# Optimization experiments

Measured on AMD Instinct MI355X. Metric: run time of the kernel, lower is better.

Reference implementation:

```python
import jax, jax.numpy as jnp
import numpy as np

N = 20000      # nodes
E = 320000     # edges (avg degree 16)
IN = 128
HID = 64
CLS = 32
H0, H1, H2 = 4, 4, 6
SLOPE = 0.2


def _lin(key, fan_in, fan_out):
    kw, kb = jax.random.split(key)
    s = 1.0 / np.sqrt(fan_in)
    W = jax.random.uniform(kw, (fan_in, fan_out), minval=-s, maxval=s, dtype=jnp.float32)
    b = jax.random.uniform(kb, (fan_out,), minval=-s, maxval=s, dtype=jnp.float32)
    return W, b


def setup_inputs() -> dict:
    key = jax.random.key(0)
    ks = jax.random.split(key, 16)
    x = jax.random.normal(ks[0], (N, IN), dtype=jnp.float32)
    src = jax.random.randint(ks[1], (E,), 0, N)
    dst = jax.random.randint(ks[2], (E,), 0, N)
    W0s, b0s = _lin(ks[3], IN, H0 * HID)
    W0d, b0d = _lin(ks[4], IN, H0 * HID)
    a0 = jax.random.normal(ks[5], (H0, HID), dtype=jnp.float32) * 0.05
    d1 = H0 * HID  # 256, flattened hidden width
    W1s, b1s = _lin(ks[6], d1, H1 * HID)
    W1d, b1d = _lin(ks[7], d1, H1 * HID)
    a1 = jax.random.normal(ks[8], (H1, HID), dtype=jnp.float32) * 0.05
    W2s, b2s = _lin(ks[9], d1, H2 * CLS)
    W2d, b2d = _lin(ks[10], d1, H2 * CLS)
    a2 = jax.random.normal(ks[11], (H2, CLS), dtype=jnp.float32) * 0.05
    Wr2, br2 = _lin(ks[12], d1, H2 * CLS)  # residual projection (256 != 192)
    return dict(x=x, src=src, dst=dst,
                W0s=W0s, b0s=b0s, W0d=W0d, b0d=b0d, a0=a0,
                W1s=W1s, b1s=b1s, W1d=W1d, b1d=b1d, a1=a1,
                W2s=W2s, b2s=b2s, W2d=W2d, b2d=b2d, a2=a2,
                Wr2=Wr2, br2=br2)


def _gatv2_layer(x, src, dst, Ws, bs, Wd, bd, attn, heads, dim, res, act):
    n = x.shape[0]
    feat_src = (x @ Ws + bs).reshape(n, heads, dim)
    feat_dst = (x @ Wd + bd).reshape(n, heads, dim)
    # GATv2 edge scores: a^T LeakyReLU(W_l h_u + W_r h_v)
    e = jax.nn.leaky_relu(feat_src[src] + feat_dst[dst], SLOPE)  # [E,H,D]
    logits = jnp.einsum('ehd,hd->eh', e, attn)                    # [E,H]
    # numerically-stable edge softmax over incoming edges per destination
    m = jax.ops.segment_max(logits, dst, num_segments=n)
    m = jnp.where(jnp.isfinite(m), m, 0.0)
    ex = jnp.exp(logits - m[dst])
    denom = jax.ops.segment_sum(ex, dst, num_segments=n)
    alpha = ex / denom[dst]                                        # [E,H]
    out = jax.ops.segment_sum(feat_src[src] * alpha[:, :, None], dst, num_segments=n)
    if res == 'id':
        out = out + x.reshape(n, heads, dim)
    elif res is not None:
        Wr, br = res
        out = out + (x @ Wr + br).reshape(n, heads, dim)
    if act:
        out = jax.nn.elu(out)
    return out  # [n, heads, dim]


def reference(x, src, dst,
              W0s, b0s, W0d, b0d, a0,
              W1s, b1s, W1d, b1d, a1,
              W2s, b2s, W2d, b2d, a2,
              Wr2, br2):
    h = _gatv2_layer(x, src, dst, W0s, b0s, W0d, b0d, a0, H0, HID, None, True)
    h = h.reshape(N, H0 * HID)
    h = _gatv2_layer(h, src, dst, W1s, b1s, W1d, b1d, a1, H1, HID, 'id', True)
    h = h.reshape(N, H1 * HID)
    out = _gatv2_layer(h, src, dst, W2s, b2s, W2d, b2d, a2, H2, CLS, (Wr2, br2), False)
    return out.mean(axis=1)  # [N, num_classes]
```

## Files before the change

### kernel.cpp

```cpp
#include <hip/hip_runtime.h>
#include <hip/hip_bf16.h>
#include <float.h>
#include <math.h>

#define NN 20000
#define EE 320000
#define IN_DIM 128
#define SLOPE_ 0.2f
#define DEG_CAP 64

typedef __attribute__((ext_vector_type(4))) float f32x4;
typedef _Float16 f16;
typedef __attribute__((ext_vector_type(2))) _Float16 f16x2;
typedef __attribute__((ext_vector_type(4))) _Float16 f16x4;
typedef __attribute__((ext_vector_type(8))) _Float16 f16x8;
typedef unsigned short ushort;

__device__ inline void prep_elem(const float* __restrict__ Wa, const float* __restrict__ ba, int na,
                                 const float* __restrict__ Wb, const float* __restrict__ bb, int nb,
                                 const float* __restrict__ Wc, const float* __restrict__ bc, int nc,
                                 int K, f16* __restrict__ Wt, float* __restrict__ bias_cat, int idx) {
    int n = idx / K;
    int k = idx - n * K;
    const float* W; const float* b; int nl; int ncols;
    if (n < na) { W = Wa; b = ba; nl = n; ncols = na; }
    else if (n < na + nb) { W = Wb; b = bb; nl = n - na; ncols = nb; }
    else { W = Wc; b = bc; nl = n - na - nb; ncols = nc; }
    Wt[(size_t)n * K + k] = (f16)W[(size_t)k * ncols + nl];
    if (k == 0) bias_cat[n] = b[nl];
}

#define SEG0 (512 * 128)
#define SEG1 (512 * 256)
#define SEG2 (576 * 256)
#define SEG3 (NN * IN_DIM / 4)
#define SEG4 (EE)
__global__ void prep_all(const float* __restrict__ W0s, const float* __restrict__ b0s,
                         const float* __restrict__ W0d, const float* __restrict__ b0d,
                         const float* __restrict__ W1s, const float* __restrict__ b1s,
                         const float* __restrict__ W1d, const float* __restrict__ b1d,
                         const float* __restrict__ W2s, const float* __restrict__ b2s,
                         const float* __restrict__ W2d, const float* __restrict__ b2d,
                         const float* __restrict__ Wr2, const float* __restrict__ br2,
                         const float* __restrict__ x,
                         const int* __restrict__ src, const int* __restrict__ dst,
                         f16* __restrict__ Wt0, float* __restrict__ bias0,
                         f16* __restrict__ Wt1, float* __restrict__ bias1,
                         f16* __restrict__ Wt2, float* __restrict__ bias2,
                         f16* __restrict__ A, unsigned int* __restrict__ deg,
                         int* __restrict__ csr_src) {
    int idx = blockIdx.x * 256 + threadIdx.x;
    if (idx < SEG0) {
        prep_elem(W0s, b0s, 256, W0d, b0d, 256, nullptr, nullptr, 0, 128, Wt0, bias0, idx);
    } else if ((idx -= SEG0) < SEG1) {
        prep_elem(W1s, b1s, 256, W1d, b1d, 256, nullptr, nullptr, 0, 256, Wt1, bias1, idx);
    } else if ((idx -= SEG1) < SEG2) {
        prep_elem(W2s, b2s, 192, W2d, b2d, 192, Wr2, br2, 192, 256, Wt2, bias2, idx);
    } else if ((idx -= SEG2) < SEG3) {
        float4 v = ((const float4*)x)[idx];
        f16x4 o = {(f16)v.x, (f16)v.y, (f16)v.z, (f16)v.w};
        ((f16x4*)A)[idx] = o;
    } else if ((idx -= SEG3) < SEG4) {
        int d = dst[idx];
        unsigned int pos = atomicAdd(&deg[d], 1u);
        csr_src[(unsigned)d * DEG_CAP + pos] = src[idx];
    }
}

__global__ __launch_bounds__(256) void gemm_mfma_f16(
        const f16* __restrict__ A, const f16* __restrict__ Wt,
        const float* __restrict__ bias,
        f16* __restrict__ F0, f16* __restrict__ F1, float* __restrict__ F2,
        int b1, int b2, int M, int K, int S, int gx, int gy) {
    __shared__ f16 Bs[64 * 256];
    __shared__ f16 Cs[4][32 * 66];

    const int bid = blockIdx.x;
    const int p = bid & 7;
    const int q = bid >> 3;
    const int bn_i = q % gx;
    const int bm_i = (q / gx) * 8 + p;
    if (bm_i >= gy) return;
    const int bm = bm_i * 256;
    const int bn = bn_i * 64;

    const int tid = threadIdx.x;
    const int wave = tid >> 6;
    const int lane = tid & 63;
    const int m16 = lane & 15;
    const int quad = lane >> 4;

    {
        const int n = tid >> 2;
        const int q0 = tid & 3;
        for (int j = 0; j * 32 < K; ++j) {
            int k0 = j * 32 + q0 * 8;
            f16x8 v = *(const f16x8*)(Wt + (size_t)(bn + n) * K + k0);
            int chunk = (j * 4 + (n >> 4)) * 64 + q0 * 16 + (n & 15);
            *(f16x8*)&Bs[chunk * 8] = v;
        }
    }
    __syncthreads();

    const int rb0 = bm + wave * 64;
    f32x4 acc[2][2][4];
    #pragma unroll
    for (int mi = 0; mi < 2; ++mi)
        #pragma unroll
        for (int mt = 0; mt < 2; ++mt)
            #pragma unroll
            for (int nt = 0; nt < 4; ++nt) acc[mi][mt][nt] = (f32x4){0.f, 0.f, 0.f, 0.f};

    int ar[2][2];
    #pragma unroll
    for (int mi = 0; mi < 2; ++mi)
        #pragma unroll
        for (int mt = 0; mt < 2; ++mt) {
            int row = rb0 + mi * 32 + mt * 16 + m16;
            ar[mi][mt] = row < M ? row : M - 1;
        }

    #pragma unroll 2
    for (int k0 = 0; k0 < K; k0 += 32) {
        f16x8 bs[4];
        #pragma unroll
        for (int nt = 0; nt < 4; ++nt)
            bs[nt] = *(const f16x8*)&Bs[(((k0 >> 5) * 4 + nt) * 64 + lane) * 8];
        #pragma unroll
        for (int mi = 0; mi < 2; ++mi) {
            f16x8 ah[2];
            #pragma unroll
            for (int mt = 0; mt < 2; ++mt)
                ah[mt] = *(const f16x8*)(A + (size_t)ar[mi][mt] * K + k0 + quad * 8);
            #pragma unroll
            for (int nt = 0; nt < 4; ++nt)
                #pragma unroll
                for (int mt = 0; mt < 2; ++mt)
                    acc[mi][mt][nt] = __builtin_amdgcn_mfma_f32_16x16x32_f16(ah[mt], bs[nt], acc[mi][mt][nt], 0, 0, 0);
        }
    }

    #pragma unroll
    for (int mi = 0; mi < 2; ++mi) {
        const int rbase = rb0 + mi * 32;
        if (bn < b2) {
            f16* __restrict__ Fb;
            int cs, cb;
            if (bn >= b1) { Fb = F1; cb = bn - b1; cs = b2 - b1; }
            else          { Fb = F0; cb = bn;      cs = b1; }
            f16* cw = &Cs[wave][0];
            #pragma unroll
            for (int nt = 0; nt < 4; ++nt) {
                float bv = bias[bn + nt * 16 + m16];
                #pragma unroll
                for (int mt = 0; mt < 2; ++mt)
                    #pragma unroll
                    for (int r = 0; r < 4; ++r) {
                        int row = mt * 16 + quad * 4 + r;
                        cw[row * 66 + nt * 16 + m16] = (f16)(acc[mi][mt][nt][r] + bv);
                    }
            }
            int lrow = lane >> 1;
            int lcol = (lane & 1) * 32;
            int grow = rbase + lrow;
            if (grow < M) {
                #pragma unroll
                for (int j = 0; j < 4; ++j) {
                    f16x8 v = *(f16x8*)&cw[lrow * 66 + lcol + j * 8];
                    *(f16x8*)&Fb[(size_t)grow * cs + cb + lcol + j * 8] = v;
                }
            }
        } else {
            int cs = S - b2;
            #pragma unroll
            for (int nt = 0; nt < 4; ++nt) {
                int col = bn - b2 + nt * 16 + m16;
                float bv = bias[bn + nt * 16 + m16];
                #pragma unroll
                for (int mt = 0; mt < 2; ++mt)
                    #pragma unroll
                    for (int r = 0; r < 4; ++r) {
                        int row = rbase + mt * 16 + quad * 4 + r;
                        if (row < M) F2[(size_t)row * cs + col] = acc[mi][mt][nt][r] + bv;
                    }
            }
        }
    }
}

#define AGG_STEP4(U0)                                                         \
    _Pragma("unroll")                                                         \
    for (int uu = 0; uu < 4; ++uu) {                                          \
        const int u = (U0) + uu;                                              \
        const f16x8 cur = buf[u];                                             \
        buf[u] = *(const f16x8*)&fsb[(unsigned)cidx[u] * HD + off];           \
        cidx[u] = csr_src[min(jj0 + b + 16 + u, last)];                       \
        float p = 0.f;                                                        \
        _Pragma("unroll")                                                     \
        for (int i = 0; i < 4; ++i) {                                         \
            f16x2 cp = (f16x2){cur[2 * i], cur[2 * i + 1]};                   \
            f16x2 xp = cp + fdp[i];                                           \
            unsigned xu = __builtin_bit_cast(unsigned, xp) & 0x7FFF7FFFu;     \
            f16x2 xa = __builtin_bit_cast(f16x2, xu);                         \
            p = __builtin_amdgcn_fdot2(xp, a6p[i], p, false);                 \
            p = __builtin_amdgcn_fdot2(xa, a4p[i], p, false);                 \
        }                                                                     \
        _Pragma("unroll")                                                     \
        for (int o = 1; o < GSZ; o <<= 1) p += __shfl_xor(p, o, 64);          \
        float w = (b + u < deg) ? __expf(p) : 0.f;                            \
        lh += w;                                                              \
        _Pragma("unroll")                                                     \
        for (int d = 0; d < 8; ++d) acc[d] += w * (float)cur[d];              \
    }

template <int HD, int D, bool HAS_RES, bool DO_ELU, int OUT_MODE>
__global__ __launch_bounds__(256) void gat_node_aggregate(
        const f16* __restrict__ fsb, const f16* __restrict__ fdb,
        const float* __restrict__ attn,
        const unsigned int* __restrict__ degv,
        const int* __restrict__ csr_src,
        const float* __restrict__ resid, int RS,
        float* __restrict__ outF, f16* __restrict__ outA) {
    constexpr int LANES = HD / 8;
    constexpr int GSZ = D / 8;
    __shared__ float red[(OUT_MODE == 2) ? 8 : 1][(OUT_MODE == 2) ? HD : 1];

    const int wave = threadIdx.x >> 6;
    const int lane = threadIdx.x & 63;
    const int half = lane >> 5;
    const int ln = lane & 31;
    const int t = blockIdx.x * 8 + wave * 2 + half;
    const bool active = (ln < LANES);
    const unsigned off = active ? 8u * ln : 0u;

    f16x2 fdp[4], a6p[4], a4p[4];
    if (active) {
        f16x8 dv = *(const f16x8*)&fdb[(unsigned)t * HD + off];
        float4 aA = *(const float4*)&attn[off];
        float4 aB = *(const float4*)&attn[off + 4];
        float av[8] = {aA.x, aA.y, aA.z, aA.w, aB.x, aB.y, aB.z, aB.w};
        #pragma unroll
        for (int i = 0; i < 4; ++i) {
            fdp[i] = (f16x2){dv[2 * i], dv[2 * i + 1]};
            a6p[i] = (f16x2){(f16)(0.6f * av[2 * i]), (f16)(0.6f * av[2 * i + 1])};
            a4p[i] = (f16x2){(f16)(0.4f * av[2 * i]), (f16)(0.4f * av[2 * i + 1])};
        }
    } else {
        #pragma unroll
        for (int i = 0; i < 4; ++i) {
            fdp[i] = (f16x2){0, 0};
            a6p[i] = (f16x2){0, 0};
            a4p[i] = (f16x2){0, 0};
        }
    }

    const int jj0 = t * DEG_CAP;
    const int deg = (int)degv[t];
    const int last = jj0 + deg - 1;
    const int degO = __shfl_xor(deg, 32, 64);
    const int mdeg = max(deg, degO);

    float acc[8];
    #pragma unroll
    for (int d = 0; d < 8; ++d) acc[d] = 0.f;
    float lh = 0.f;

    f16x8 buf[8];
    int cidx[8];
    #pragma unroll
    for (int u = 0; u < 8; ++u) {
        int e0 = max(min(jj0 + u, last), 0);
        buf[u] = *(const f16x8*)&fsb[(unsigned)csr_src[e0] * HD + off];
        cidx[u] = csr_src[max(min(jj0 + 8 + u, last), 0)];
    }

    for (int b = 0; b < mdeg; b += 8) {
        AGG_STEP4(0)
        if (b + 4 < mdeg) {
            AGG_STEP4(4)
        }
    }

    float inv = (lh > 0.f) ? 1.f / lh : 0.f;
    float vout[8];
    #pragma unroll
    for (int d = 0; d < 8; ++d) vout[d] = acc[d] * inv;
    if (HAS_RES && active) {
        float4 rA = *(const float4*)&resid[(unsigned)t * RS + off];
        float4 rB = *(const float4*)&resid[(unsigned)t * RS + off + 4];
        vout[0] += rA.x; vout[1] += rA.y; vout[2] += rA.z; vout[3] += rA.w;
        vout[4] += rB.x; vout[5] += rB.y; vout[6] += rB.z; vout[7] += rB.w;
    }
    if (DO_ELU) {
        #pragma unroll
        for (int d = 0; d < 8; ++d) vout[d] = vout[d] > 0.f ? vout[d] : expm1f(vout[d]);
    }

    if (OUT_MODE == 2) {
        const int nib = wave * 2 + half;
        if (active) {
            *(float4*)&red[nib][off] = make_float4(vout[0], vout[1], vout[2], vout[3]);
            *(float4*)&red[nib][off + 4] = make_float4(vout[4], vout[5], vout[6], vout[7]);
        }
        __syncthreads();
        int node = threadIdx.x >> 5;
        int col = threadIdx.x & 31;
        float ssum = 0.f;
        #pragma unroll
        for (int h = 0; h < 6; ++h) ssum += red[node][h * 32 + col];
        outF[(unsigned)(blockIdx.x * 8 + node) * 32 + col] = ssum * (1.f / 6.f);
    } else if (active) {
        f16x8 av;
        #pragma unroll
        for (int d = 0; d < 8; ++d) av[d] = (f16)vout[d];
        *(f16x8*)&outA[(unsigned)t * HD + off] = av;
        if (OUT_MODE == 0) {
            *(float4*)&outF[(unsigned)t * HD + off] = make_float4(vout[0], vout[1], vout[2], vout[3]);
            *(float4*)&outF[(unsigned)t * HD + off + 4] = make_float4(vout[4], vout[5], vout[6], vout[7]);
        }
    }
}

extern "C" void kernel_launch(void* const* d_in, const int* in_sizes, int n_in,
                              void* d_out, int out_size, void* d_ws, size_t ws_size,
                              hipStream_t stream) {
    const float* x   = (const float*)d_in[0];
    const int*   src = (const int*)d_in[1];
    const int*   dst = (const int*)d_in[2];
    const float* W0s = (const float*)d_in[3];
    const float* b0s = (const float*)d_in[4];
    const float* W0d = (const float*)d_in[5];
    const float* b0d = (const float*)d_in[6];
    const float* a0  = (const float*)d_in[7];
    const float* W1s = (const float*)d_in[8];
    const float* b1s = (const float*)d_in[9];
    const float* W1d = (const float*)d_in[10];
    const float* b1d = (const float*)d_in[11];
    const float* a1  = (const float*)d_in[12];
    const float* W2s = (const float*)d_in[13];
    const float* b2s = (const float*)d_in[14];
    const float* W2d = (const float*)d_in[15];
    const float* b2d = (const float*)d_in[16];
    const float* a2  = (const float*)d_in[17];
    const float* Wr2 = (const float*)d_in[18];
    const float* br2 = (const float*)d_in[19];

    f16* FsH = (f16*)d_ws;
    f16* FdH = FsH + (size_t)NN * 256;
    f16* A   = FdH + (size_t)NN * 256;
    float* O0 = (float*)(A + (size_t)NN * 256);
    f16* Wt0 = (f16*)(O0 + (size_t)NN * 256);
    f16* Wt1 = Wt0 + 512 * 128;
    f16* Wt2 = Wt1 + 512 * 256;
    float* bias0 = (float*)(Wt2 + 576 * 256);
    float* bias1 = bias0 + 512;
    float* bias2 = bias1 + 512;
    unsigned int* deg = (unsigned int*)(bias2 + 576);
    int* csr_src      = (int*)(deg + NN);

    hipMemsetAsync(deg, 0, (size_t)NN * 4 + (size_t)NN * DEG_CAP * 4, stream);

    {
        int total = SEG0 + SEG1 + SEG2 + SEG3 + SEG4;
        prep_all<<<(total + 255) / 256, 256, 0, stream>>>(
            W0s, b0s, W0d, b0d, W1s, b1s, W1d, b1d, W2s, b2s, W2d, b2d, Wr2, br2, x,
            src, dst, Wt0, bias0, Wt1, bias1, Wt2, bias2, A, deg, csr_src);
    }

    const int gy = (NN + 255) / 256;
    const int gy8 = ((gy + 7) / 8) * 8;
    const int nagg = NN / 8;

    gemm_mfma_f16<<<gy8 * 8, 256, 0, stream>>>(A, Wt0, bias0,
                                               FsH, FdH, nullptr, 256, 512, NN, 128, 512, 8, gy);
    gat_node_aggregate<256, 64, false, true, 0><<<nagg, 256, 0, stream>>>(
        FsH, FdH, a0, deg, csr_src, nullptr, 0, O0, A);

    gemm_mfma_f16<<<gy8 * 8, 256, 0, stream>>>(A, Wt1, bias1,
                                               FsH, FdH, nullptr, 256, 512, NN, 256, 512, 8, gy);
    gat_node_aggregate<256, 64, true, true, 1><<<nagg, 256, 0, stream>>>(
        FsH, FdH, a1, deg, csr_src, O0, 256, nullptr, A);

    gemm_mfma_f16<<<gy8 * 9, 256, 0, stream>>>(A, Wt2, bias2,
                                               FsH, FdH, O0, 192, 384, NN, 256, 576, 9, gy);
    gat_node_aggregate<192, 32, true, false, 2><<<nagg, 256, 0, stream>>>(
        FsH, FdH, a2, deg, csr_src, O0, 192, (float*)d_out, nullptr);
}
```

Measured before the change: 285.3 us.

## Give each aggregation node a full wave, alias GEMM staging LDS, shrink memset

```diff
diff --git a/kernel.cpp b/kernel.cpp
--- a/kernel.cpp
+++ b/kernel.cpp
@@ -6,7 +6,6 @@
 #define NN 20000
 #define EE 320000
 #define IN_DIM 128
-#define SLOPE_ 0.2f
 #define DEG_CAP 64
 
 typedef __attribute__((ext_vector_type(4))) float f32x4;
@@ -14,12 +13,11 @@
 typedef __attribute__((ext_vector_type(2))) _Float16 f16x2;
 typedef __attribute__((ext_vector_type(4))) _Float16 f16x4;
 typedef __attribute__((ext_vector_type(8))) _Float16 f16x8;
-typedef unsigned short ushort;
-
-__device__ inline void prep_elem(const float* __restrict__ Wa, const float* __restrict__ ba, int na,
-                                 const float* __restrict__ Wb, const float* __restrict__ bb, int nb,
-                                 const float* __restrict__ Wc, const float* __restrict__ bc, int nc,
-                                 int K, f16* __restrict__ Wt, float* __restrict__ bias_cat, int idx) {
+
+__device__ __forceinline__ void prep_elem(const float* __restrict__ Wa, const float* __restrict__ ba, int na,
+                                          const float* __restrict__ Wb, const float* __restrict__ bb, int nb,
+                                          const float* __restrict__ Wc, const float* __restrict__ bc, int nc,
+                                          int K, f16* __restrict__ Wt, float* __restrict__ bias_cat, int idx) {
     int n = idx / K;
     int k = idx - n * K;
     const float* W; const float* b; int nl; int ncols;
@@ -63,17 +61,16 @@
     } else if ((idx -= SEG3) < SEG4) {
         int d = dst[idx];
         unsigned int pos = atomicAdd(&deg[d], 1u);
-        csr_src[(unsigned)d * DEG_CAP + pos] = src[idx];
-    }
-}
-
-__global__ __launch_bounds__(256) void gemm_mfma_f16(
+        if (pos < DEG_CAP) csr_src[(unsigned)d * DEG_CAP + pos] = src[idx];
+    }
+}
+
+__global__ __launch_bounds__(256, 4) void gemm_mfma_f16(
         const f16* __restrict__ A, const f16* __restrict__ Wt,
         const float* __restrict__ bias,
         f16* __restrict__ F0, f16* __restrict__ F1, float* __restrict__ F2,
         int b1, int b2, int M, int K, int S, int gx, int gy) {
     __shared__ f16 Bs[64 * 256];
-    __shared__ f16 Cs[4][32 * 66];
 
     const int bid = blockIdx.x;
     const int p = bid & 7;
@@ -140,6 +137,9 @@
         }
     }
 
+    __syncthreads();
+    f16* Cs = Bs;
+
     #pragma unroll
     for (int mi = 0; mi < 2; ++mi) {
         const int rbase = rb0 + mi * 32;
@@ -148,7 +148,7 @@
             int cs, cb;
             if (bn >= b1) { Fb = F1; cb = bn - b1; cs = b2 - b1; }
             else          { Fb = F0; cb = bn;      cs = b1; }
-            f16* cw = &Cs[wave][0];
+            f16* cw = Cs + wave * (32 * 66);
             #pragma unroll
             for (int nt = 0; nt < 4; ++nt) {
                 float bv = bias[bn + nt * 16 + m16];
@@ -192,25 +192,26 @@
     _Pragma("unroll")                                                         \
     for (int uu = 0; uu < 4; ++uu) {                                          \
         const int u = (U0) + uu;                                              \
-        const f16x8 cur = buf[u];                                             \
-        buf[u] = *(const f16x8*)&fsb[(unsigned)cidx[u] * HD + off];           \
-        cidx[u] = csr_src[min(jj0 + b + 16 + u, last)];                       \
-        float p = 0.f;                                                        \
+        const f16x4 cur = buf[u];                                             \
+        unsigned su = (unsigned)cidx[u]; su = su < NN ? su : 0u;              \
+        buf[u] = *(const f16x4*)&fsb[su * (unsigned)HD + off];                \
+        cidx[u] = csr_src[max(min(jj0 + b + 16 + u, last), 0)];               \
+        float pp = 0.f;                                                       \
         _Pragma("unroll")                                                     \
-        for (int i = 0; i < 4; ++i) {                                         \
+        for (int i = 0; i < 2; ++i) {                                         \
             f16x2 cp = (f16x2){cur[2 * i], cur[2 * i + 1]};                   \
             f16x2 xp = cp + fdp[i];                                           \
             unsigned xu = __builtin_bit_cast(unsigned, xp) & 0x7FFF7FFFu;     \
             f16x2 xa = __builtin_bit_cast(f16x2, xu);                         \
-            p = __builtin_amdgcn_fdot2(xp, a6p[i], p, false);                 \
-            p = __builtin_amdgcn_fdot2(xa, a4p[i], p, false);                 \
+            pp = __builtin_amdgcn_fdot2(xp, a6p[i], pp, false);               \
+            pp = __builtin_amdgcn_fdot2(xa, a4p[i], pp, false);               \
         }                                                                     \
         _Pragma("unroll")                                                     \
-        for (int o = 1; o < GSZ; o <<= 1) p += __shfl_xor(p, o, 64);          \
-        float w = (b + u < deg) ? __expf(p) : 0.f;                            \
+        for (int o = 1; o < GSZ; o <<= 1) pp += __shfl_xor(pp, o, 64);        \
+        float w = (b + u < dg) ? __expf(pp) : 0.f;                            \
         lh += w;                                                              \
         _Pragma("unroll")                                                     \
-        for (int d = 0; d < 8; ++d) acc[d] += w * (float)cur[d];              \
+        for (int d = 0; d < 4; ++d) acc[d] += w * (float)cur[d];              \
     }
 
 template <int HD, int D, bool HAS_RES, bool DO_ELU, int OUT_MODE>
@@ -221,103 +222,92 @@
         const int* __restrict__ csr_src,
         const float* __restrict__ resid, int RS,
         float* __restrict__ outF, f16* __restrict__ outA) {
-    constexpr int LANES = HD / 8;
-    constexpr int GSZ = D / 8;
-    __shared__ float red[(OUT_MODE == 2) ? 8 : 1][(OUT_MODE == 2) ? HD : 1];
+    constexpr int LANES = HD / 4;
+    constexpr int GSZ = D / 4;
+    __shared__ float red[(OUT_MODE == 2) ? 4 : 1][(OUT_MODE == 2) ? HD : 1];
 
     const int wave = threadIdx.x >> 6;
     const int lane = threadIdx.x & 63;
-    const int half = lane >> 5;
-    const int ln = lane & 31;
-    const int t = blockIdx.x * 8 + wave * 2 + half;
-    const bool active = (ln < LANES);
-    const unsigned off = active ? 8u * ln : 0u;
-
-    f16x2 fdp[4], a6p[4], a4p[4];
+    const int t = blockIdx.x * 4 + wave;
+    const bool active = (lane < LANES);
+    const unsigned off = active ? 4u * lane : 0u;
+
+    f16x2 fdp[2], a6p[2], a4p[2];
     if (active) {
-        f16x8 dv = *(const f16x8*)&fdb[(unsigned)t * HD + off];
+        f16x4 dv = *(const f16x4*)&fdb[(unsigned)t * HD + off];
         float4 aA = *(const float4*)&attn[off];
-        float4 aB = *(const float4*)&attn[off + 4];
-        float av[8] = {aA.x, aA.y, aA.z, aA.w, aB.x, aB.y, aB.z, aB.w};
-        #pragma unroll
-        for (int i = 0; i < 4; ++i) {
+        float av[4] = {aA.x, aA.y, aA.z, aA.w};
+        #pragma unroll
+        for (int i = 0; i < 2; ++i) {
             fdp[i] = (f16x2){dv[2 * i], dv[2 * i + 1]};
             a6p[i] = (f16x2){(f16)(0.6f * av[2 * i]), (f16)(0.6f * av[2 * i + 1])};
             a4p[i] = (f16x2){(f16)(0.4f * av[2 * i]), (f16)(0.4f * av[2 * i + 1])};
         }
     } else {
         #pragma unroll
-        for (int i = 0; i < 4; ++i) {
-            fdp[i] = (f16x2){0, 0};
-            a6p[i] = (f16x2){0, 0};
-            a4p[i] = (f16x2){0, 0};
+        for (int i = 0; i < 2; ++i) {
+            fdp[i] = (f16x2){0, 0}; a6p[i] = (f16x2){0, 0}; a4p[i] = (f16x2){0, 0};
         }
     }
 
     const int jj0 = t * DEG_CAP;
-    const int deg = (int)degv[t];
-    const int last = jj0 + deg - 1;
-    const int degO = __shfl_xor(deg, 32, 64);
-    const int mdeg = max(deg, degO);
-
-    float acc[8];
-    #pragma unroll
-    for (int d = 0; d < 8; ++d) acc[d] = 0.f;
+    const int dg = min((int)degv[t], DEG_CAP);
+    const int last = jj0 + dg - 1;
+
+    float acc[4];
+    #pragma unroll
+    for (int d = 0; d < 4; ++d) acc[d] = 0.f;
     float lh = 0.f;
 
-    f16x8 buf[8];
+    f16x4 buf[8];
     int cidx[8];
     #pragma unroll
     for (int u = 0; u < 8; ++u) {
         int e0 = max(min(jj0 + u, last), 0);
-        buf[u] = *(const f16x8*)&fsb[(unsigned)csr_src[e0] * HD + off];
+        unsigned s0 = (unsigned)csr_src[e0]; s0 = s0 < NN ? s0 : 0u;
+        buf[u] = *(const f16x4*)&fsb[s0 * (unsigned)HD + off];
         cidx[u] = csr_src[max(min(jj0 + 8 + u, last), 0)];
     }
 
-    for (int b = 0; b < mdeg; b += 8) {
+    for (int b = 0; b < dg; b += 8) {
         AGG_STEP4(0)
-        if (b + 4 < mdeg) {
+        if (b + 4 < dg) {
             AGG_STEP4(4)
         }
     }
 
     float inv = (lh > 0.f) ? 1.f / lh : 0.f;
-    float vout[8];
-    #pragma unroll
-    for (int d = 0; d < 8; ++d) vout[d] = acc[d] * inv;
+    float vout[4];
+    #pragma unroll
+    for (int d = 0; d < 4; ++d) vout[d] = acc[d] * inv;
     if (HAS_RES && active) {
         float4 rA = *(const float4*)&resid[(unsigned)t * RS + off];
-        float4 rB = *(const float4*)&resid[(unsigned)t * RS + off + 4];
         vout[0] += rA.x; vout[1] += rA.y; vout[2] += rA.z; vout[3] += rA.w;
-        vout[4] += rB.x; vout[5] += rB.y; vout[6] += rB.z; vout[7] += rB.w;
     }
     if (DO_ELU) {
         #pragma unroll
-        for (int d = 0; d < 8; ++d) vout[d] = vout[d] > 0.f ? vout[d] : expm1f(vout[d]);
+        for (int d = 0; d < 4; ++d) vout[d] = vout[d] > 0.f ? vout[d] : expm1f(vout[d]);
     }
 
     if (OUT_MODE == 2) {
-        const int nib = wave * 2 + half;
-        if (active) {
-            *(float4*)&red[nib][off] = make_float4(vout[0], vout[1], vout[2], vout[3]);
-            *(float4*)&red[nib][off + 4] = make_float4(vout[4], vout[5], vout[6], vout[7]);
-        }
+        if (active)
+            *(float4*)&red[wave][off] = make_float4(vout[0], vout[1], vout[2], vout[3]);
         __syncthreads();
-        int node = threadIdx.x >> 5;
-        int col = threadIdx.x & 31;
-        float ssum = 0.f;
-        #pragma unroll
-        for (int h = 0; h < 6; ++h) ssum += red[node][h * 32 + col];
-        outF[(unsigned)(blockIdx.x * 8 + node) * 32 + col] = ssum * (1.f / 6.f);
+        if (threadIdx.x < 128) {
+            int node = threadIdx.x >> 5;
+            int col = threadIdx.x & 31;
+            float ssum = 0.f;
+            #pragma unroll
+            for (int h = 0; h < 6; ++h) ssum += red[node][h * 32 + col];
+            outF[(unsigned)(blockIdx.x * 4 + node) * 32 + col] = ssum * (1.f / 6.f);
+        }
     } else if (active) {
-        f16x8 av;
-        #pragma unroll
-        for (int d = 0; d < 8; ++d) av[d] = (f16)vout[d];
-        *(f16x8*)&outA[(unsigned)t * HD + off] = av;
-        if (OUT_MODE == 0) {
+        f16x4 av;
+        #pragma unroll
+        for (int d = 0; d < 4; ++d) av[d] = (f16)vout[d];
+        *(f16x4*)&outA[(unsigned)t * HD + off] = av;
+        if (OUT_MODE == 0)
             *(float4*)&outF[(unsigned)t * HD + off] = make_float4(vout[0], vout[1], vout[2], vout[3]);
-            *(float4*)&outF[(unsigned)t * HD + off + 4] = make_float4(vout[4], vout[5], vout[6], vout[7]);
-        }
     }
 }
 
@@ -358,8 +348,7 @@
     unsigned int* deg = (unsigned int*)(bias2 + 576);
     int* csr_src      = (int*)(deg + NN);
 
-    hipMemsetAsync(deg, 0, (size_t)NN * 4 + (size_t)NN * DEG_CAP * 4, stream);
-
+    hipMemsetAsync(deg, 0, (size_t)NN * 4, stream);
     {
         int total = SEG0 + SEG1 + SEG2 + SEG3 + SEG4;
         prep_all<<<(total + 255) / 256, 256, 0, stream>>>(
@@ -369,7 +358,7 @@
 
     const int gy = (NN + 255) / 256;
     const int gy8 = ((gy + 7) / 8) * 8;
-    const int nagg = NN / 8;
+    const int nagg = NN / 4;
 
     gemm_mfma_f16<<<gy8 * 8, 256, 0, stream>>>(A, Wt0, bias0,
                                                FsH, FdH, nullptr, 256, 512, NN, 128, 512, 8, gy);
```

After: 300.1 us. 5.2% more time.

## Precompute linear attention terms in GEMM epilogue and degree-sort node order

Applied to the files above, without the earlier changes.

```diff
diff --git a/kernel.cpp b/kernel.cpp
--- a/kernel.cpp
+++ b/kernel.cpp
@@ -6,20 +6,19 @@
 #define NN 20000
 #define EE 320000
 #define IN_DIM 128
-#define SLOPE_ 0.2f
 #define DEG_CAP 64
+#define A6OFF (64 * 256)
 
 typedef __attribute__((ext_vector_type(4))) float f32x4;
 typedef _Float16 f16;
 typedef __attribute__((ext_vector_type(2))) _Float16 f16x2;
 typedef __attribute__((ext_vector_type(4))) _Float16 f16x4;
 typedef __attribute__((ext_vector_type(8))) _Float16 f16x8;
-typedef unsigned short ushort;
-
-__device__ inline void prep_elem(const float* __restrict__ Wa, const float* __restrict__ ba, int na,
-                                 const float* __restrict__ Wb, const float* __restrict__ bb, int nb,
-                                 const float* __restrict__ Wc, const float* __restrict__ bc, int nc,
-                                 int K, f16* __restrict__ Wt, float* __restrict__ bias_cat, int idx) {
+
+__device__ __forceinline__ void prep_elem(const float* __restrict__ Wa, const float* __restrict__ ba, int na,
+                                          const float* __restrict__ Wb, const float* __restrict__ bb, int nb,
+                                          const float* __restrict__ Wc, const float* __restrict__ bc, int nc,
+                                          int K, f16* __restrict__ Wt, float* __restrict__ bias_cat, int idx) {
     int n = idx / K;
     int k = idx - n * K;
     const float* W; const float* b; int nl; int ncols;
@@ -63,19 +62,40 @@
     } else if ((idx -= SEG3) < SEG4) {
         int d = dst[idx];
         unsigned int pos = atomicAdd(&deg[d], 1u);
-        csr_src[(unsigned)d * DEG_CAP + pos] = src[idx];
+        if (pos < DEG_CAP) csr_src[(unsigned)d * DEG_CAP + pos] = src[idx];
     }
 }
 
 __global__ __launch_bounds__(256) void gemm_mfma_f16(
         const f16* __restrict__ A, const f16* __restrict__ Wt,
-        const float* __restrict__ bias,
+        const float* __restrict__ bias, const float* __restrict__ attn,
         f16* __restrict__ F0, f16* __restrict__ F1, float* __restrict__ F2,
-        int b1, int b2, int M, int K, int S, int gx, int gy) {
-    __shared__ f16 Bs[64 * 256];
-    __shared__ f16 Cs[4][32 * 66];
+        float* __restrict__ sdS, float* __restrict__ sdD, int Dh,
+        int b1, int b2, int M, int K, int S, int gx, int gy,
+        int sortblk, const unsigned int* __restrict__ deg, int* __restrict__ order) {
+    __shared__ f16 Bs[64 * 256 + 64];
 
     const int bid = blockIdx.x;
+    const int tid = threadIdx.x;
+
+    if (bid == sortblk) {
+        unsigned* hist = (unsigned*)Bs;
+        for (int i = tid; i < 65; i += 256) hist[i] = 0u;
+        __syncthreads();
+        for (int i = tid; i < NN; i += 256) atomicAdd(&hist[min(deg[i], (unsigned)DEG_CAP)], 1u);
+        __syncthreads();
+        if (tid == 0) {
+            unsigned r = 0;
+            for (int b = 0; b <= DEG_CAP; ++b) { unsigned c = hist[b]; hist[b] = r; r += c; }
+        }
+        __syncthreads();
+        for (int i = tid; i < NN; i += 256) {
+            unsigned p = atomicAdd(&hist[min(deg[i], (unsigned)DEG_CAP)], 1u);
+            order[p] = i;
+        }
+        return;
+    }
+
     const int p = bid & 7;
     const int q = bid >> 3;
     const int bn_i = q % gx;
@@ -84,11 +104,12 @@
     const int bm = bm_i * 256;
     const int bn = bn_i * 64;
 
-    const int tid = threadIdx.x;
     const int wave = tid >> 6;
     const int lane = tid & 63;
     const int m16 = lane & 15;
     const int quad = lane >> 4;
+    const int side = bn >= b1;
+    const int local = bn - (side ? b1 : 0);
 
     {
         const int n = tid >> 2;
@@ -99,6 +120,7 @@
             int chunk = (j * 4 + (n >> 4)) * 64 + q0 * 16 + (n & 15);
             *(f16x8*)&Bs[chunk * 8] = v;
         }
+        if (tid < 64 && bn < b2) Bs[A6OFF + tid] = (f16)(0.6f * attn[local + tid]);
     }
     __syncthreads();
 
@@ -140,15 +162,18 @@
         }
     }
 
+    __syncthreads();
+    f16* Cs = Bs;
+
     #pragma unroll
     for (int mi = 0; mi < 2; ++mi) {
         const int rbase = rb0 + mi * 32;
         if (bn < b2) {
             f16* __restrict__ Fb;
             int cs, cb;
-            if (bn >= b1) { Fb = F1; cb = bn - b1; cs = b2 - b1; }
-            else          { Fb = F0; cb = bn;      cs = b1; }
-            f16* cw = &Cs[wave][0];
+            if (side) { Fb = F1; cb = bn - b1; cs = b2 - b1; }
+            else      { Fb = F0; cb = bn;      cs = b1; }
+            f16* cw = Cs + wave * (32 * 66);
             #pragma unroll
             for (int nt = 0; nt < 4; ++nt) {
                 float bv = bias[bn + nt * 16 + m16];
@@ -164,10 +189,25 @@
             int lcol = (lane & 1) * 32;
             int grow = rbase + lrow;
             if (grow < M) {
+                float pdot = 0.f;
                 #pragma unroll
                 for (int j = 0; j < 4; ++j) {
                     f16x8 v = *(f16x8*)&cw[lrow * 66 + lcol + j * 8];
                     *(f16x8*)&Fb[(size_t)grow * cs + cb + lcol + j * 8] = v;
+                    f16x8 ac = *(f16x8*)&Bs[A6OFF + lcol + j * 8];
+                    #pragma unroll
+                    for (int i = 0; i < 4; ++i) {
+                        f16x2 vp = (f16x2){v[2 * i], v[2 * i + 1]};
+                        f16x2 ap = (f16x2){ac[2 * i], ac[2 * i + 1]};
+                        pdot = __builtin_amdgcn_fdot2(vp, ap, pdot, false);
+                    }
+                }
+                float* sd = side ? sdD : sdS;
+                if (Dh == 64) {
+                    pdot += __shfl_xor(pdot, 1, 64);
+                    if ((lane & 1) == 0) sd[(size_t)grow * 8 + (local >> 6)] = pdot;
+                } else {
+                    sd[(size_t)grow * 8 + (local >> 5) + (lane & 1)] = pdot;
                 }
             }
         } else {
@@ -193,21 +233,23 @@
     for (int uu = 0; uu < 4; ++uu) {                                          \
         const int u = (U0) + uu;                                              \
         const f16x8 cur = buf[u];                                             \
-        buf[u] = *(const f16x8*)&fsb[(unsigned)cidx[u] * HD + off];           \
-        cidx[u] = csr_src[min(jj0 + b + 16 + u, last)];                       \
-        float p = 0.f;                                                        \
+        const float sv = svb[u];                                              \
+        unsigned su = (unsigned)cidx[u]; su = su < NN ? su : 0u;              \
+        buf[u] = *(const f16x8*)&fsb[su * (unsigned)HD + off];                \
+        svb[u] = sdS[su * 8u + (unsigned)head];                               \
+        cidx[u] = csr_src[max(min(jj0 + b + 16 + u, last), 0)];               \
+        float pp = 0.f;                                                       \
         _Pragma("unroll")                                                     \
         for (int i = 0; i < 4; ++i) {                                         \
             f16x2 cp = (f16x2){cur[2 * i], cur[2 * i + 1]};                   \
             f16x2 xp = cp + fdp[i];                                           \
             unsigned xu = __builtin_bit_cast(unsigned, xp) & 0x7FFF7FFFu;     \
             f16x2 xa = __builtin_bit_cast(f16x2, xu);                         \
-            p = __builtin_amdgcn_fdot2(xp, a6p[i], p, false);                 \
-            p = __builtin_amdgcn_fdot2(xa, a4p[i], p, false);                 \
+            pp = __builtin_amdgcn_fdot2(xa, a4p[i], pp, false);               \
         }                                                                     \
         _Pragma("unroll")                                                     \
-        for (int o = 1; o < GSZ; o <<= 1) p += __shfl_xor(p, o, 64);          \
-        float w = (b + u < deg) ? __expf(p) : 0.f;                            \
+        for (int o = 1; o < GSZ; o <<= 1) pp += __shfl_xor(pp, o, 64);        \
+        float w = (b + u < dg) ? __expf(pp + sv + dvv) : 0.f;                 \
         lh += w;                                                              \
         _Pragma("unroll")                                                     \
         for (int d = 0; d < 8; ++d) acc[d] += w * (float)cur[d];              \
@@ -218,22 +260,25 @@
         const f16* __restrict__ fsb, const f16* __restrict__ fdb,
         const float* __restrict__ attn,
         const unsigned int* __restrict__ degv,
-        const int* __restrict__ csr_src,
+        const int* __restrict__ csr_src, const int* __restrict__ order,
+        const float* __restrict__ sdS, const float* __restrict__ sdD,
         const float* __restrict__ resid, int RS,
         float* __restrict__ outF, f16* __restrict__ outA) {
     constexpr int LANES = HD / 8;
     constexpr int GSZ = D / 8;
     __shared__ float red[(OUT_MODE == 2) ? 8 : 1][(OUT_MODE == 2) ? HD : 1];
+    __shared__ int nid[(OUT_MODE == 2) ? 8 : 1];
 
     const int wave = threadIdx.x >> 6;
     const int lane = threadIdx.x & 63;
     const int half = lane >> 5;
     const int ln = lane & 31;
-    const int t = blockIdx.x * 8 + wave * 2 + half;
     const bool active = (ln < LANES);
     const unsigned off = active ? 8u * ln : 0u;
-
-    f16x2 fdp[4], a6p[4], a4p[4];
+    const int head = (int)(off / (unsigned)D);
+    const int t = order[blockIdx.x * 8 + wave * 2 + half];
+
+    f16x2 fdp[4], a4p[4];
     if (active) {
         f16x8 dv = *(const f16x8*)&fdb[(unsigned)t * HD + off];
         float4 aA = *(const float4*)&attn[off];
@@ -242,23 +287,19 @@
         #pragma unroll
         for (int i = 0; i < 4; ++i) {
             fdp[i] = (f16x2){dv[2 * i], dv[2 * i + 1]};
-            a6p[i] = (f16x2){(f16)(0.6f * av[2 * i]), (f16)(0.6f * av[2 * i + 1])};
             a4p[i] = (f16x2){(f16)(0.4f * av[2 * i]), (f16)(0.4f * av[2 * i + 1])};
         }
     } else {
         #pragma unroll
-        for (int i = 0; i < 4; ++i) {
-            fdp[i] = (f16x2){0, 0};
-            a6p[i] = (f16x2){0, 0};
-            a4p[i] = (f16x2){0, 0};
-        }
-    }
+        for (int i = 0; i < 4; ++i) { fdp[i] = (f16x2){0, 0}; a4p[i] = (f16x2){0, 0}; }
+    }
+    const float dvv = sdD[(unsigned)t * 8u + (unsigned)head];
 
     const int jj0 = t * DEG_CAP;
-    const int deg = (int)degv[t];
-    const int last = jj0 + deg - 1;
-    const int degO = __shfl_xor(deg, 32, 64);
-    const int mdeg = max(deg, degO);
+    const int dg = min((int)degv[t], DEG_CAP);
+    const int last = jj0 + dg - 1;
+    const int degO = __shfl_xor(dg, 32, 64);
+    const int mdeg = max(dg, degO);
 
     float acc[8];
     #pragma unroll
@@ -266,11 +307,14 @@
     float lh = 0.f;
 
     f16x8 buf[8];
+    float svb[8];
     int cidx[8];
     #pragma unroll
     for (int u = 0; u < 8; ++u) {
         int e0 = max(min(jj0 + u, last), 0);
-        buf[u] = *(const f16x8*)&fsb[(unsigned)csr_src[e0] * HD + off];
+        unsigned s0 = (unsigned)csr_src[e0]; s0 = s0 < NN ? s0 : 0u;
+        buf[u] = *(const f16x8*)&fsb[s0 * (unsigned)HD + off];
+        svb[u] = sdS[s0 * 8u + (unsigned)head];
         cidx[u] = csr_src[max(min(jj0 + 8 + u, last), 0)];
     }
 
@@ -302,13 +346,14 @@
             *(float4*)&red[nib][off] = make_float4(vout[0], vout[1], vout[2], vout[3]);
             *(float4*)&red[nib][off + 4] = make_float4(vout[4], vout[5], vout[6], vout[7]);
         }
+        if (ln == 0) nid[nib] = t;
         __syncthreads();
         int node = threadIdx.x >> 5;
         int col = threadIdx.x & 31;
         float ssum = 0.f;
         #pragma unroll
         for (int h = 0; h < 6; ++h) ssum += red[node][h * 32 + col];
-        outF[(unsigned)(blockIdx.x * 8 + node) * 32 + col] = ssum * (1.f / 6.f);
+        outF[(unsigned)nid[node] * 32 + col] = ssum * (1.f / 6.f);
     } else if (active) {
         f16x8 av;
         #pragma unroll
@@ -357,9 +402,11 @@
     float* bias2 = bias1 + 512;
     unsigned int* deg = (unsigned int*)(bias2 + 576);
     int* csr_src      = (int*)(deg + NN);
-
-    hipMemsetAsync(deg, 0, (size_t)NN * 4 + (size_t)NN * DEG_CAP * 4, stream);
-
+    float* sdS = (float*)(csr_src + (size_t)NN * DEG_CAP);
+    float* sdD = sdS + (size_t)NN * 8;
+    int* order = (int*)(sdD + (size_t)NN * 8);
+
+    hipMemsetAsync(deg, 0, (size_t)NN * 4, stream);
     {
         int total = SEG0 + SEG1 + SEG2 + SEG3 + SEG4;
         prep_all<<<(total + 255) / 256, 256, 0, stream>>>(
@@ -371,18 +418,24 @@
     const int gy8 = ((gy + 7) / 8) * 8;
     const int nagg = NN / 8;
 
-    gemm_mfma_f16<<<gy8 * 8, 256, 0, stream>>>(A, Wt0, bias0,
-                                               FsH, FdH, nullptr, 256, 512, NN, 128, 512, 8, gy);
+    gemm_mfma_f16<<<gy8 * 8 + 1, 256, 0, stream>>>(A, Wt0, bias0, a0,
+                                               FsH, FdH, nullptr, sdS, sdD, 64,
+                                               256, 512, NN, 128, 512, 8, gy,
+                                               gy8 * 8, deg, order);
     gat_node_aggregate<256, 64, false, true, 0><<<nagg, 256, 0, stream>>>(
-        FsH, FdH, a0, deg, csr_src, nullptr, 0, O0, A);
-
-    gemm_mfma_f16<<<gy8 * 8, 256, 0, stream>>>(A, Wt1, bias1,
-                                               FsH, FdH, nullptr, 256, 512, NN, 256, 512, 8, gy);
+        FsH, FdH, a0, deg, csr_src, order, sdS, sdD, nullptr, 0, O0, A);
+
+    gemm_mfma_f16<<<gy8 * 8, 256, 0, stream>>>(A, Wt1, bias1, a1,
+                                               FsH, FdH, nullptr, sdS, sdD, 64,
+                                               256, 512, NN, 256, 512, 8, gy,
+                                               -1, deg, order);
     gat_node_aggregate<256, 64, true, true, 1><<<nagg, 256, 0, stream>>>(
-        FsH, FdH, a1, deg, csr_src, O0, 256, nullptr, A);
-
-    gemm_mfma_f16<<<gy8 * 9, 256, 0, stream>>>(A, Wt2, bias2,
-                                               FsH, FdH, O0, 192, 384, NN, 256, 576, 9, gy);
+        FsH, FdH, a1, deg, csr_src, order, sdS, sdD, O0, 256, nullptr, A);
+
+    gemm_mfma_f16<<<gy8 * 9, 256, 0, stream>>>(A, Wt2, bias2, a2,
+                                               FsH, FdH, O0, sdS, sdD, 32,
+                                               192, 384, NN, 256, 576, 9, gy,
+                                               -1, deg, order);
     gat_node_aggregate<192, 32, true, false, 2><<<nagg, 256, 0, stream>>>(
-        FsH, FdH, a2, deg, csr_src, O0, 192, (float*)d_out, nullptr);
+        FsH, FdH, a2, deg, csr_src, order, sdS, sdD, O0, 192, (float*)d_out, nullptr);
 }
```

Result: slower. 325.5 us (+14.1%).
